# Optimization experiments

Hardware: AMD Instinct MI355X
Metric: run time of the kernel (lower is better)

The kernel has to match this reference:

```python
import jax, jax.numpy as jnp
import numpy as np

E, K, N, T = 8, 2048, 1024, 4096


def setup_inputs() -> dict:
    key = jax.random.key(0)
    kx, kw = jax.random.split(key)
    x = jax.random.normal(kx, (T, K), dtype=jnp.float32)
    weight = jax.random.normal(kw, (E, N, K), dtype=jnp.float32)
    # cumulative group end offsets per expert; equal split, offs[-1] == T
    offs = (jnp.arange(1, E + 1) * (T // E)).astype(jnp.int32)
    return {"x": x, "weight": weight, "offs": offs}


def reference(x, weight, offs):
    # torch: wt = weight.transpose(-2, -1); y = torch._grouped_mm(x, wt, offs)
    # Grouped GEMM over contiguous ragged token groups: tokens in
    # [starts[e], offs[e]) are multiplied by expert e's weight.
    wt = jnp.swapaxes(weight, -2, -1)  # [E, K, N]
    starts = jnp.concatenate([jnp.zeros((1,), offs.dtype), offs[:-1]])  # [E]
    tok = jnp.arange(x.shape[0], dtype=offs.dtype)[:, None]  # [T, 1]
    y = jnp.zeros((x.shape[0], wt.shape[-1]), dtype=x.dtype)
    for e in range(wt.shape[0]):  # fixed small expert count
        mask = (tok >= starts[e]) & (tok < offs[e])  # [T, 1]
        y = y + jnp.where(mask, x, jnp.zeros((), x.dtype)) @ wt[e]
    return y
```

## Files before the change

kernel.cpp:

```cpp
#include <hip/hip_runtime.h>
#include <hip/hip_bf16.h>

typedef __attribute__((ext_vector_type(4))) float f32x4;
typedef __attribute__((ext_vector_type(4))) unsigned int u32x4;
typedef __attribute__((ext_vector_type(8))) __bf16 bf16x8;

namespace {
constexpr int T_ = 4096;
constexpr int K_ = 2048;
constexpr int N_ = 1024;
constexpr int E_ = 8;
constexpr int BM = 128, BN = 128, BK = 32;
constexpr int KSPLIT = 2;
constexpr int KHALF = K_ / KSPLIT;
constexpr int NKS = KHALF / BK;
constexpr int LSTR = BK + 8;
constexpr size_t PART_ELEMS = (size_t)T_ * N_;
}

__device__ __forceinline__ unsigned int pk2(float a, float b) {
    union { __hip_bfloat162 h; unsigned int u; } c;
    c.h = __float22bfloat162_rn(make_float2(a, b));
    return c.u;
}

__device__ __forceinline__ u32x4 cvt8(f32x4 a, f32x4 b) {
    u32x4 r;
    r.x = pk2(a.x, a.y);
    r.y = pk2(a.z, a.w);
    r.z = pk2(b.x, b.y);
    r.w = pk2(b.z, b.w);
    return r;
}

template <int ATOMIC>
__global__ __launch_bounds__(256, 2) void gg_bf16_kernel(
        const float* __restrict__ x, const float* __restrict__ w,
        const int* __restrict__ offs, float* __restrict__ out) {
    __shared__ __align__(16) unsigned short As[2][BM * LSTR];
    __shared__ __align__(16) unsigned short Bs[2][BN * LSTR];

    const int tid = threadIdx.x;
    const int lane = tid & 63;
    const int wid = tid >> 6;
    const int wr = wid >> 1, wc = wid & 1;

    const int b = blockIdx.x;
    const int xcd = b & 7;
    const int inner = b >> 3;
    const int ks = inner >> 5;
    const int rem = inner & 31;
    const int by = xcd * 4 + (rem >> 3);
    const int bx = rem & 7;
    const int brow = by * BM;
    const int bcol = bx * BN;
    const int k0 = ks * KHALF;

    float* outp = ATOMIC ? out : (out + (size_t)ks * PART_ELEMS);

    const int srow = tid >> 2;
    const int scol = (tid & 3) * 8;
    const float* aB0 = x + (size_t)(brow + srow) * K_ + k0 + scol;
    const float* aB1 = aB0 + (size_t)64 * K_;
    const int ldsO0 = srow * LSTR + scol;
    const int ldsO1 = (srow + 64) * LSTR + scol;

    const int frow = lane & 15;
    const int fk = (lane >> 4) * 8;
    const int aF = (wr * 64 + frow) * LSTR + fk;
    const int bF = (wc * 64 + frow) * LSTR + fk;

#define LOADT(t)                                                      \
    do {                                                              \
        const float* _a0 = aB0 + (t) * BK;                            \
        const float* _a1 = aB1 + (t) * BK;                            \
        const float* _b0 = bB0 + (t) * BK;                            \
        const float* _b1 = bB1 + (t) * BK;                            \
        ra0 = *(const f32x4*)_a0; ra1 = *(const f32x4*)(_a0 + 4);     \
        ra2 = *(const f32x4*)_a1; ra3 = *(const f32x4*)(_a1 + 4);     \
        rb0 = *(const f32x4*)_b0; rb1 = *(const f32x4*)(_b0 + 4);     \
        rb2 = *(const f32x4*)_b1; rb3 = *(const f32x4*)(_b1 + 4);     \
    } while (0)

#define STORET(buf)                                                   \
    do {                                                              \
        *(u32x4*)&As[buf][ldsO0] = cvt8(ra0, ra1);                    \
        *(u32x4*)&As[buf][ldsO1] = cvt8(ra2, ra3);                    \
        *(u32x4*)&Bs[buf][ldsO0] = cvt8(rb0, rb1);                    \
        *(u32x4*)&Bs[buf][ldsO1] = cvt8(rb2, rb3);                    \
    } while (0)

    for (int e = 0; e < E_; ++e) {
        const int s = (e == 0) ? 0 : offs[e - 1];
        const int en = offs[e];
        if (en <= brow || s >= brow + BM) continue;

        const float* bB0 = w + ((size_t)e * N_ + bcol + srow) * K_ + k0 + scol;
        const float* bB1 = bB0 + (size_t)64 * K_;

        f32x4 ra0, ra1, ra2, ra3, rb0, rb1, rb2, rb3;
        LOADT(0);
        STORET(0);
        __syncthreads();

        f32x4 acc[4][4];
#pragma unroll
        for (int m = 0; m < 4; ++m)
#pragma unroll
            for (int n = 0; n < 4; ++n)
                acc[m][n] = f32x4{0.0f, 0.0f, 0.0f, 0.0f};

        for (int t = 0; t < NKS; ++t) {
            const int cur = t & 1;
            if (t + 1 < NKS) LOADT(t + 1);
            bf16x8 af[4], bg[4];
#pragma unroll
            for (int m = 0; m < 4; ++m)
                af[m] = *(const bf16x8*)&As[cur][aF + m * 16 * LSTR];
#pragma unroll
            for (int n = 0; n < 4; ++n)
                bg[n] = *(const bf16x8*)&Bs[cur][bF + n * 16 * LSTR];
#pragma unroll
            for (int m = 0; m < 4; ++m)
#pragma unroll
                for (int n = 0; n < 4; ++n)
                    acc[m][n] = __builtin_amdgcn_mfma_f32_16x16x32_bf16(
                        af[m], bg[n], acc[m][n], 0, 0, 0);
            if (t + 1 < NKS) STORET(cur ^ 1);
            __syncthreads();
        }

        const int cb = bcol + wc * 64 + frow;
#pragma unroll
        for (int m = 0; m < 4; ++m) {
            const int r0 = brow + wr * 64 + m * 16 + (lane >> 4) * 4;
#pragma unroll
            for (int r = 0; r < 4; ++r) {
                const int row = r0 + r;
                if (row < s || row >= en) continue;
                float* yp = outp + (size_t)row * N_ + cb;
#pragma unroll
                for (int n = 0; n < 4; ++n) {
                    if (ATOMIC) atomicAdd(&yp[n * 16], acc[m][n][r]);
                    else        yp[n * 16] = acc[m][n][r];
                }
            }
        }
        __syncthreads();
    }
#undef LOADT
#undef STORET
}

__global__ __launch_bounds__(256) void gg_reduce_kernel(
        const float* __restrict__ part, float* __restrict__ y) {
    const size_t i = (size_t)blockIdx.x * blockDim.x + threadIdx.x;
    const f32x4 a = ((const f32x4*)part)[i];
    const f32x4 b = ((const f32x4*)(part + PART_ELEMS))[i];
    ((f32x4*)y)[i] = a + b;
}

extern "C" void kernel_launch(void* const* d_in, const int* in_sizes, int n_in,
                              void* d_out, int out_size, void* d_ws, size_t ws_size,
                              hipStream_t stream) {
    const float* x = (const float*)d_in[0];
    const float* w = (const float*)d_in[1];
    const int* offs = (const int*)d_in[2];
    float* y = (float*)d_out;
    const int grid = (T_ / BM) * (N_ / BN) * KSPLIT;

    if (ws_size >= KSPLIT * PART_ELEMS * sizeof(float)) {
        float* part = (float*)d_ws;
        gg_bf16_kernel<0><<<dim3(grid), dim3(256), 0, stream>>>(x, w, offs, part);
        gg_reduce_kernel<<<dim3((int)(PART_ELEMS / 4 / 256)), dim3(256), 0, stream>>>(part, y);
    } else {
        hipMemsetAsync(d_out, 0, PART_ELEMS * sizeof(float), stream);
        gg_bf16_kernel<1><<<dim3(grid), dim3(256), 0, stream>>>(x, w, offs, y);
    }
}
```

Baseline: 49.84 us.

## Raise split-K to four, deepen register prefetch, and raise occupancy hint

```diff
diff --git a/kernel.cpp b/kernel.cpp
--- a/kernel.cpp
+++ b/kernel.cpp
@@ -11,9 +11,6 @@
 constexpr int N_ = 1024;
 constexpr int E_ = 8;
 constexpr int BM = 128, BN = 128, BK = 32;
-constexpr int KSPLIT = 2;
-constexpr int KHALF = K_ / KSPLIT;
-constexpr int NKS = KHALF / BK;
 constexpr int LSTR = BK + 8;
 constexpr size_t PART_ELEMS = (size_t)T_ * N_;
 }
@@ -33,10 +30,12 @@
     return r;
 }
 
-template <int ATOMIC>
-__global__ __launch_bounds__(256, 2) void gg_bf16_kernel(
+template <int KSPLIT, int ATOMIC>
+__global__ __launch_bounds__(256, 4) void gg_bf16_kernel(
         const float* __restrict__ x, const float* __restrict__ w,
         const int* __restrict__ offs, float* __restrict__ out) {
+    constexpr int KCH = K_ / KSPLIT;
+    constexpr int NKS = KCH / BK;
     __shared__ __align__(16) unsigned short As[2][BM * LSTR];
     __shared__ __align__(16) unsigned short Bs[2][BN * LSTR];
 
@@ -54,7 +53,7 @@
     const int bx = rem & 7;
     const int brow = by * BM;
     const int bcol = bx * BN;
-    const int k0 = ks * KHALF;
+    const int k0 = ks * KCH;
 
     float* outp = ATOMIC ? out : (out + (size_t)ks * PART_ELEMS);
 
@@ -101,6 +100,7 @@
         f32x4 ra0, ra1, ra2, ra3, rb0, rb1, rb2, rb3;
         LOADT(0);
         STORET(0);
+        LOADT(1);
         __syncthreads();
 
         f32x4 acc[4][4];
@@ -112,7 +112,8 @@
 
         for (int t = 0; t < NKS; ++t) {
             const int cur = t & 1;
-            if (t + 1 < NKS) LOADT(t + 1);
+            if (t + 1 < NKS) STORET(cur ^ 1);
+            if (t + 2 < NKS) LOADT(t + 2);
             bf16x8 af[4], bg[4];
 #pragma unroll
             for (int m = 0; m < 4; ++m)
@@ -126,7 +127,6 @@
                 for (int n = 0; n < 4; ++n)
                     acc[m][n] = __builtin_amdgcn_mfma_f32_16x16x32_bf16(
                         af[m], bg[n], acc[m][n], 0, 0, 0);
-            if (t + 1 < NKS) STORET(cur ^ 1);
             __syncthreads();
         }
 
@@ -152,12 +152,15 @@
 #undef STORET
 }
 
+template <int P>
 __global__ __launch_bounds__(256) void gg_reduce_kernel(
         const float* __restrict__ part, float* __restrict__ y) {
     const size_t i = (size_t)blockIdx.x * blockDim.x + threadIdx.x;
-    const f32x4 a = ((const f32x4*)part)[i];
-    const f32x4 b = ((const f32x4*)(part + PART_ELEMS))[i];
-    ((f32x4*)y)[i] = a + b;
+    f32x4 acc = ((const f32x4*)part)[i];
+#pragma unroll
+    for (int p = 1; p < P; ++p)
+        acc += ((const f32x4*)(part + (size_t)p * PART_ELEMS))[i];
+    ((f32x4*)y)[i] = acc;
 }
 
 extern "C" void kernel_launch(void* const* d_in, const int* in_sizes, int n_in,
@@ -167,14 +170,17 @@
     const float* w = (const float*)d_in[1];
     const int* offs = (const int*)d_in[2];
     float* y = (float*)d_out;
-    const int grid = (T_ / BM) * (N_ / BN) * KSPLIT;
+    float* part = (float*)d_ws;
+    const int rgrid = (int)(PART_ELEMS / 4 / 256);
 
-    if (ws_size >= KSPLIT * PART_ELEMS * sizeof(float)) {
-        float* part = (float*)d_ws;
-        gg_bf16_kernel<0><<<dim3(grid), dim3(256), 0, stream>>>(x, w, offs, part);
-        gg_reduce_kernel<<<dim3((int)(PART_ELEMS / 4 / 256)), dim3(256), 0, stream>>>(part, y);
+    if (ws_size >= 4 * PART_ELEMS * sizeof(float)) {
+        gg_bf16_kernel<4, 0><<<dim3(256 * 4), dim3(256), 0, stream>>>(x, w, offs, part);
+        gg_reduce_kernel<4><<<dim3(rgrid), dim3(256), 0, stream>>>(part, y);
+    } else if (ws_size >= 2 * PART_ELEMS * sizeof(float)) {
+        gg_bf16_kernel<2, 0><<<dim3(256 * 2), dim3(256), 0, stream>>>(x, w, offs, part);
+        gg_reduce_kernel<2><<<dim3(rgrid), dim3(256), 0, stream>>>(part, y);
     } else {
         hipMemsetAsync(d_out, 0, PART_ELEMS * sizeof(float), stream);
-        gg_bf16_kernel<1><<<dim3(grid), dim3(256), 0, stream>>>(x, w, offs, y);
+        gg_bf16_kernel<2, 1><<<dim3(256 * 2), dim3(256), 0, stream>>>(x, w, offs, y);
     }
 }
```

Measured after the change: 62.84 us. +26.1%, slower.
